# Kernel optimization log

Measured on AMD Instinct MI355X. Metric: run time of the kernel, lower is better.

Reference implementation:

```python
import jax, jax.numpy as jnp
import numpy as np

TOPK = 13
ALPHA = 1.0
BETA = 6.0
EPS = 1e-9


def _make_boxes(key, shape, img=640.0, min_sz=10.0, max_sz=110.0):
    k1, k2 = jax.random.split(key)
    cxcy = jax.random.uniform(k1, shape[:-1] + (2,)) * img
    wh = min_sz + jax.random.uniform(k2, shape[:-1] + (2,)) * (max_sz - min_sz)
    return jnp.concatenate([cxcy - wh / 2, cxcy + wh / 2], axis=-1)


def setup_inputs() -> dict:
    key = jax.random.key(0)
    ks = jax.random.split(key, 8)
    B, L, C, n, K = 16, 8400, 1, 32, 68
    pred_scores = jax.random.uniform(ks[0], (B, L, C))
    pred_bboxes = _make_boxes(ks[1], (B, L, 4))
    anchor_points = jax.random.uniform(ks[2], (L, 2)) * 640.0
    gt_labels = jax.random.randint(ks[3], (B, n, 1), 0, C).astype(jnp.int64)
    gt_bboxes = _make_boxes(ks[4], (B, n, 4))
    gt_poses = jax.random.normal(ks[5], (B, n, K, 3))
    gt_vertices = jax.random.normal(ks[6], (B, n, K, 3))
    gt_rotations = jax.random.normal(ks[7], (B, n, 3, 3))
    pad_gt_mask = jnp.ones((B, n, 1), jnp.float32)
    return {"pred_scores": pred_scores, "pred_bboxes": pred_bboxes,
            "anchor_points": anchor_points, "gt_labels": gt_labels,
            "gt_bboxes": gt_bboxes, "gt_poses": gt_poses,
            "gt_vertices": gt_vertices, "gt_rotations": gt_rotations,
            "pad_gt_mask": pad_gt_mask, "bg_index": 1}


def batch_iou_similarity(box1, box2):
    # box1 [B,n,4], box2 [B,L,4] -> [B,n,L]
    b1 = box1[:, :, None, :]
    b2 = box2[:, None, :, :]
    x1y1 = jnp.maximum(b1[..., :2], b2[..., :2])
    x2y2 = jnp.minimum(b1[..., 2:], b2[..., 2:])
    overlap = jnp.clip(x2y2 - x1y1, 0).prod(-1)
    area1 = jnp.clip(b1[..., 2:] - b1[..., :2], 0).prod(-1)
    area2 = jnp.clip(b2[..., 2:] - b2[..., :2], 0).prod(-1)
    return overlap / (area1 + area2 - overlap + EPS)


def check_points_inside_bboxes(points, bboxes):
    # points [L,2], bboxes [B,n,4] -> [B,n,L] float
    x = points[None, None, :, 0]
    y = points[None, None, :, 1]
    xmin, ymin, xmax, ymax = jnp.split(bboxes[:, :, None, :], 4, axis=-1)
    deltas = jnp.stack([x - xmin[..., 0], y - ymin[..., 0],
                        xmax[..., 0] - x, ymax[..., 0] - y], axis=-1)
    return (deltas.min(-1) > EPS).astype(bboxes.dtype)


def gather_topk_anchors(metrics, topk, topk_mask):
    # metrics [B,n,L], topk_mask [B,n,1] -> [B,n,L]
    L = metrics.shape[-1]
    _, topk_idxs = jax.lax.top_k(metrics, topk)  # [B,n,topk]
    is_in_topk = jax.nn.one_hot(topk_idxs, L, dtype=metrics.dtype).sum(-2)
    return is_in_topk * topk_mask


def compute_max_iou_anchor(ious):
    # [B,n,L] -> one-hot over gt dim of per-anchor argmax iou
    n = ious.shape[1]
    idx = ious.argmax(axis=1)  # [B,L]
    return jnp.transpose(jax.nn.one_hot(idx, n, dtype=ious.dtype), (0, 2, 1))


def reference(pred_scores, pred_bboxes, anchor_points, gt_labels, gt_bboxes,
              gt_poses, gt_vertices, gt_rotations, pad_gt_mask, bg_index):
    B, L, C = pred_scores.shape
    n = gt_bboxes.shape[1]
    K = gt_poses.shape[2]

    ious = batch_iou_similarity(gt_bboxes, pred_bboxes)  # [B,n,L]
    ps_t = jnp.transpose(pred_scores, (0, 2, 1))  # [B,C,L]
    lbl = gt_labels[..., 0]  # [B,n]
    bbox_cls_scores = jnp.take_along_axis(ps_t, lbl[:, :, None], axis=1)  # [B,n,L]

    alignment_metrics = (bbox_cls_scores ** ALPHA) * (ious ** BETA)
    is_in_gts = check_points_inside_bboxes(anchor_points, gt_bboxes)
    is_in_topk = gather_topk_anchors(alignment_metrics * is_in_gts, TOPK, pad_gt_mask)
    mask_positive = is_in_topk * is_in_gts * pad_gt_mask  # [B,n,L]
    mask_positive_sum = mask_positive.sum(axis=1)  # [B,L]

    # resolve anchors assigned to multiple gts by max IoU (no-op when none)
    mask_multiple = jnp.broadcast_to((mask_positive_sum[:, None, :] > 1), mask_positive.shape)
    is_max_iou = compute_max_iou_anchor(ious)
    mask_positive = jnp.where(mask_multiple, is_max_iou, mask_positive)
    mask_positive_sum = mask_positive.sum(axis=1)

    batch_ind = jnp.arange(B, dtype=jnp.int32)[:, None]
    assigned_gt_index = mask_positive.argmax(axis=1)  # [B,L]
    assigned_gt_index = assigned_gt_index + batch_ind * n
    flat_idx = assigned_gt_index.reshape(-1)

    assigned_labels = gt_labels.reshape(-1)[flat_idx].reshape(B, L)
    assigned_labels = jnp.where(mask_positive_sum > 0, assigned_labels, bg_index)

    assigned_bboxes = gt_bboxes.reshape(-1, 4)[flat_idx].reshape(B, L, 4)
    assigned_poses = gt_poses.reshape(-1, K, 3)[flat_idx].reshape(B, L, K, 3)
    assigned_vertices = gt_vertices.reshape(-1, K, 3)[flat_idx].reshape(B, L, K, 3)
    assigned_rotations = gt_rotations.reshape(-1, 3, 3)[flat_idx].reshape(B, L, 3, 3)

    scores_oh = jax.nn.one_hot(assigned_labels, C + 1, dtype=pred_scores.dtype)
    keep = jnp.array([i for i in range(C + 1) if i != bg_index], dtype=jnp.int32)
    assigned_scores = scores_oh[..., keep]  # [B,L,C]

    am = alignment_metrics * mask_positive
    max_metrics_per_instance = am.max(axis=-1, keepdims=True)
    max_ious_per_instance = (ious * mask_positive).max(axis=-1, keepdims=True)
    am = am / (max_metrics_per_instance + EPS) * max_ious_per_instance
    am = am.max(axis=1)[:, :, None]  # [B,L,1]
    assigned_scores = assigned_scores * am

    return (assigned_labels, assigned_bboxes, assigned_scores, assigned_poses,
            assigned_vertices, assigned_rotations, assigned_gt_index)
```

## Files before the change

kernel.cpp:

```cpp
#include <hip/hip_runtime.h>

#define Bn 16
#define Ln 8400
#define Cn 1
#define Ngt 32
#define Kpt 68
#define TOPKN 13
#define EPSF 1e-9f

typedef unsigned int u32;

#define OFF_LABELS   0
#define OFF_BBOXES   134400
#define OFF_SCORES   672000
#define OFF_POSES    806400
#define OFF_VERTS    28224000
#define OFF_ROT      55641600
#define OFF_GTIDX    56851200

__device__ __forceinline__ float iou_box(float gx0, float gy0, float gx1, float gy1,
                                         float4 p) {
    float ix0 = fmaxf(gx0, p.x), iy0 = fmaxf(gy0, p.y);
    float ix1 = fminf(gx1, p.z), iy1 = fminf(gy1, p.w);
    float ov = fmaxf(ix1 - ix0, 0.f) * fmaxf(iy1 - iy0, 0.f);
    float a1 = fmaxf(gx1 - gx0, 0.f) * fmaxf(gy1 - gy0, 0.f);
    float a2 = fmaxf(p.z - p.x, 0.f) * fmaxf(p.w - p.y, 0.f);
    return ov / (a1 + a2 - ov + EPSF);
}

__global__ void __launch_bounds__(256) k1_topk(
    const float* __restrict__ pred_scores, const float* __restrict__ pred_bboxes,
    const float* __restrict__ anchors, const int* __restrict__ gt_labels,
    const float* __restrict__ gt_bboxes, const float* __restrict__ pad_mask,
    u32* __restrict__ posmask)
{
    __shared__ float smet[Ln];
    __shared__ float rv[256];
    __shared__ int   ri[256];
    __shared__ int   sel[TOPKN];
    const int bi = blockIdx.x;
    const int b = bi / Ngt, i = bi % Ngt;
    const int tid = threadIdx.x;

    const float gx0 = gt_bboxes[bi*4+0];
    const float gy0 = gt_bboxes[bi*4+1];
    const float gx1 = gt_bboxes[bi*4+2];
    const float gy1 = gt_bboxes[bi*4+3];
    const int   label = gt_labels[bi];

    const float4* pb = (const float4*)(pred_bboxes + (size_t)b * Ln * 4);
    const float*  ps = pred_scores + (size_t)b * Ln * Cn;
    const float2* ap = (const float2*)anchors;

    for (int l = tid; l < Ln; l += 256) {
        float4 pv = pb[l];
        float iou = iou_box(gx0, gy0, gx1, gy1, pv);
        float sc = ps[l * Cn + label];
        float i2 = iou * iou;
        float m = sc * (i2 * i2 * i2);
        float2 av = ap[l];
        float dmin = fminf(fminf(av.x - gx0, av.y - gy0),
                           fminf(gx1 - av.x, gy1 - av.y));
        smet[l] = (dmin > EPSF) ? m : 0.0f;
    }
    __syncthreads();

    for (int t = 0; t < TOPKN; t++) {
        float bv = -1.f; int bidx = 0;
        for (int l = tid; l < Ln; l += 256) {
            float v = smet[l];
            if (v > bv) { bv = v; bidx = l; }
        }
        rv[tid] = bv; ri[tid] = bidx;
        __syncthreads();
        for (int s = 128; s > 0; s >>= 1) {
            if (tid < s) {
                float ov2 = rv[tid+s]; int oi = ri[tid+s];
                if (ov2 > rv[tid] || (ov2 == rv[tid] && oi < ri[tid])) {
                    rv[tid] = ov2; ri[tid] = oi;
                }
            }
            __syncthreads();
        }
        if (tid == 0) { sel[t] = ri[0]; smet[ri[0]] = -1.f; }
        __syncthreads();
    }

    const float pad = pad_mask[bi];
    if (tid < TOPKN && pad != 0.f) {
        int l = sel[tid];
        float2 av = ap[l];
        float dmin = fminf(fminf(av.x - gx0, av.y - gy0),
                           fminf(gx1 - av.x, gy1 - av.y));
        if (dmin > EPSF) atomicOr(&posmask[(size_t)b * Ln + l], 1u << i);
    }
}

__global__ void __launch_bounds__(256) k2_resolve(
    const float* __restrict__ pred_scores, const float* __restrict__ pred_bboxes,
    const int* __restrict__ gt_labels, const float* __restrict__ gt_bboxes,
    const u32* __restrict__ posmask, u32* __restrict__ finalmask,
    int* __restrict__ srcidx, float* __restrict__ met_sel,
    float* __restrict__ maxm, float* __restrict__ maxiou)
{
    int bl = blockIdx.x * 256 + threadIdx.x;
    if (bl >= Bn * Ln) return;
    int b = bl / Ln, l = bl - b * Ln;
    u32 pm = posmask[bl];
    u32 fm = pm;
    float4 pbox = ((const float4*)pred_bboxes)[bl];
    const float4* gb = (const float4*)(gt_bboxes + (size_t)b * Ngt * 4);
    if (__popc(pm) > 1) {
        float best = -1.f; int bi2 = 0;
        for (int i = 0; i < Ngt; i++) {
            float4 g = gb[i];
            float v = iou_box(g.x, g.y, g.z, g.w, pbox);
            if (v > best) { best = v; bi2 = i; }
        }
        fm = 1u << bi2;
    }
    finalmask[bl] = fm;
    int idx = fm ? (__ffs((int)fm) - 1) : 0;
    int src = b * Ngt + idx;
    srcidx[bl] = src;
    float met = 0.f;
    if (fm) {
        float4 g = gb[idx];
        float iou = iou_box(g.x, g.y, g.z, g.w, pbox);
        float sc = pred_scores[(size_t)bl * Cn + gt_labels[src]];
        float i2 = iou * iou;
        met = sc * (i2 * i2 * i2);
        atomicMax((int*)&maxm[src],   __float_as_int(met));
        atomicMax((int*)&maxiou[src], __float_as_int(iou));
    }
    met_sel[bl] = met;
}

__global__ void __launch_bounds__(256) k4_outputs(
    const u32* __restrict__ finalmask, const int* __restrict__ srcidx,
    const float* __restrict__ met_sel, const float* __restrict__ maxm_a,
    const float* __restrict__ maxiou_a, const int* __restrict__ gt_labels,
    const float* __restrict__ gt_bboxes, const float* __restrict__ gt_rot,
    const int* __restrict__ bg_index_p, float* __restrict__ out)
{
    int bl = blockIdx.x * 256 + threadIdx.x;
    if (bl >= Bn * Ln) return;
    const int bg = *bg_index_p;
    u32 fm = finalmask[bl];
    int src = srcidx[bl];
    int label = fm ? gt_labels[src] : bg;
    float am = 0.f;
    if (fm) am = met_sel[bl] / (maxm_a[src] + EPSF) * maxiou_a[src];
    int keep0 = (bg == 0) ? 1 : 0;
    float sc = (label == keep0) ? am : 0.f;

    out[OFF_LABELS + bl] = (float)label;
    out[OFF_SCORES + bl] = sc;
    out[OFF_GTIDX  + bl] = (float)src;
    ((float4*)(out + OFF_BBOXES))[bl] = ((const float4*)gt_bboxes)[src];
    const float* rs = gt_rot + src * 9;
    float* rd = out + OFF_ROT + (size_t)bl * 9;
#pragma unroll
    for (int j = 0; j < 9; j++) rd[j] = rs[j];
}

__global__ void __launch_bounds__(256) k5_gather(
    const float* __restrict__ gt_poses, const float* __restrict__ gt_verts,
    const int* __restrict__ srcidx, float* __restrict__ out)
{
    const int QPER = (Kpt * 3) / 4;
    const int total = Bn * Ln * QPER;
    int q = blockIdx.x * 256 + threadIdx.x;
    if (q >= 2 * total) return;
    const float* ga = gt_poses;
    float4* outp = (float4*)(out + OFF_POSES);
    int qq = q;
    if (qq >= total) { qq -= total; ga = gt_verts; outp = (float4*)(out + OFF_VERTS); }
    int bl = qq / QPER;
    int r = qq - bl * QPER;
    int src = srcidx[bl];
    outp[qq] = ((const float4*)ga)[src * QPER + r];
}

extern "C" void kernel_launch(void* const* d_in, const int* in_sizes, int n_in,
                              void* d_out, int out_size, void* d_ws, size_t ws_size,
                              hipStream_t stream)
{
    const float* pred_scores = (const float*)d_in[0];
    const float* pred_bboxes = (const float*)d_in[1];
    const float* anchors     = (const float*)d_in[2];
    const int*   gt_labels   = (const int*)d_in[3];
    const float* gt_bboxes   = (const float*)d_in[4];
    const float* gt_poses    = (const float*)d_in[5];
    const float* gt_verts    = (const float*)d_in[6];
    const float* gt_rot      = (const float*)d_in[7];
    const float* pad_mask    = (const float*)d_in[8];
    const int*   bg_index    = (const int*)d_in[9];

    const int nBL = Bn * Ln;
    u32*   posmask  = (u32*)d_ws;
    float* maxm     = (float*)(posmask + nBL);
    float* maxiou   = maxm + Bn * Ngt;
    u32*   finalmask= (u32*)(maxiou + Bn * Ngt);
    int*   srcidx   = (int*)(finalmask + nBL);
    float* met_sel  = (float*)(srcidx + nBL);

    hipMemsetAsync(posmask, 0, ((size_t)nBL + 2 * Bn * Ngt) * sizeof(u32), stream);

    k1_topk<<<Bn * Ngt, 256, 0, stream>>>(pred_scores, pred_bboxes, anchors,
                                          gt_labels, gt_bboxes, pad_mask, posmask);
    k2_resolve<<<(nBL + 255) / 256, 256, 0, stream>>>(pred_scores, pred_bboxes,
                                                      gt_labels, gt_bboxes, posmask,
                                                      finalmask, srcidx, met_sel,
                                                      maxm, maxiou);
    k4_outputs<<<(nBL + 255) / 256, 256, 0, stream>>>(finalmask, srcidx, met_sel,
                                                      maxm, maxiou, gt_labels,
                                                      gt_bboxes, gt_rot, bg_index,
                                                      (float*)d_out);
    const int nq = 2 * Bn * Ln * ((Kpt * 3) / 4);
    k5_gather<<<(nq + 255) / 256, 256, 0, stream>>>(gt_poses, gt_verts, srcidx,
                                                    (float*)d_out);
}
```

Measured before the change: 302.3 us.

## Compact in-box candidates before top-k and merge output kernels

The top-k kernel now stores only anchors that lie inside the GT box and have a positive metric, compacted into a shared list of up to 2048 entries. The 13 selection rounds then scan that short list with wavefront shuffle reductions instead of scanning all 8400 anchors with a shared-memory tree. The kernel also exits early for padded GTs and falls back to a serial index-order fill when fewer than 13 candidates exist. The two output kernels are merged into one launch. The risks are silent truncation if more than 2048 candidates appear, and subtle tie-breaking differences from the reference top_k when zero-metric anchors are involved.

```diff
diff --git a/kernel.cpp b/kernel.cpp
--- a/kernel.cpp
+++ b/kernel.cpp
@@ -7,6 +7,7 @@
 #define Kpt 68
 #define TOPKN 13
 #define EPSF 1e-9f
+#define CAP 2048
 
 typedef unsigned int u32;
 
@@ -34,13 +35,18 @@
     const float* __restrict__ gt_bboxes, const float* __restrict__ pad_mask,
     u32* __restrict__ posmask)
 {
-    __shared__ float smet[Ln];
-    __shared__ float rv[256];
-    __shared__ int   ri[256];
+    __shared__ float cmet[CAP];
+    __shared__ int   cidx[CAP];
+    __shared__ int   count;
+    __shared__ float rv[4];
+    __shared__ int   rl[4], rc[4];
     __shared__ int   sel[TOPKN];
+
     const int bi = blockIdx.x;
-    const int b = bi / Ngt, i = bi % Ngt;
+    const int b = bi >> 5, i = bi & 31;
     const int tid = threadIdx.x;
+
+    if (pad_mask[bi] == 0.f) return;
 
     const float gx0 = gt_bboxes[bi*4+0];
     const float gy0 = gt_bboxes[bi*4+1];
@@ -52,47 +58,75 @@
     const float*  ps = pred_scores + (size_t)b * Ln * Cn;
     const float2* ap = (const float2*)anchors;
 
+    if (tid == 0) count = 0;
+    __syncthreads();
+
     for (int l = tid; l < Ln; l += 256) {
-        float4 pv = pb[l];
-        float iou = iou_box(gx0, gy0, gx1, gy1, pv);
-        float sc = ps[l * Cn + label];
-        float i2 = iou * iou;
-        float m = sc * (i2 * i2 * i2);
         float2 av = ap[l];
         float dmin = fminf(fminf(av.x - gx0, av.y - gy0),
                            fminf(gx1 - av.x, gy1 - av.y));
-        smet[l] = (dmin > EPSF) ? m : 0.0f;
+        if (dmin > EPSF) {
+            float4 pv = pb[l];
+            float iou = iou_box(gx0, gy0, gx1, gy1, pv);
+            float sc = ps[l * Cn + label];
+            float i2 = iou * iou;
+            float m = sc * (i2 * i2 * i2);
+            if (m > 0.f) {
+                int c = atomicAdd(&count, 1);
+                if (c < CAP) { cmet[c] = m; cidx[c] = l; }
+            }
+        }
     }
     __syncthreads();
-
-    for (int t = 0; t < TOPKN; t++) {
-        float bv = -1.f; int bidx = 0;
-        for (int l = tid; l < Ln; l += 256) {
-            float v = smet[l];
-            if (v > bv) { bv = v; bidx = l; }
-        }
-        rv[tid] = bv; ri[tid] = bidx;
-        __syncthreads();
-        for (int s = 128; s > 0; s >>= 1) {
-            if (tid < s) {
-                float ov2 = rv[tid+s]; int oi = ri[tid+s];
-                if (ov2 > rv[tid] || (ov2 == rv[tid] && oi < ri[tid])) {
-                    rv[tid] = ov2; ri[tid] = oi;
+    int p = min(count, CAP);
+
+    if (p > TOPKN) {
+        for (int t = 0; t < TOPKN; t++) {
+            float bv = -1.f; int bl = 1 << 30, bc = 0;
+            for (int c = tid; c < p; c += 256) {
+                float v = cmet[c];
+                int l = cidx[c];
+                if (v > bv || (v == bv && l < bl)) { bv = v; bl = l; bc = c; }
+            }
+            #pragma unroll
+            for (int off = 32; off > 0; off >>= 1) {
+                float ov = __shfl_down(bv, off);
+                int ol = __shfl_down(bl, off);
+                int oc = __shfl_down(bc, off);
+                if (ov > bv || (ov == bv && ol < bl)) { bv = ov; bl = ol; bc = oc; }
+            }
+            int w = tid >> 6;
+            if ((tid & 63) == 0) { rv[w] = bv; rl[w] = bl; rc[w] = bc; }
+            __syncthreads();
+            if (tid == 0) {
+                float fv = rv[0]; int fl = rl[0], fc = rc[0];
+                #pragma unroll
+                for (int w2 = 1; w2 < 4; w2++) {
+                    if (rv[w2] > fv || (rv[w2] == fv && rl[w2] < fl)) {
+                        fv = rv[w2]; fl = rl[w2]; fc = rc[w2];
+                    }
                 }
+                sel[t] = fl;
+                cmet[fc] = -1.f;
             }
             __syncthreads();
         }
-        if (tid == 0) { sel[t] = ri[0]; smet[ri[0]] = -1.f; }
-        __syncthreads();
-    }
-
-    const float pad = pad_mask[bi];
-    if (tid < TOPKN && pad != 0.f) {
-        int l = sel[tid];
-        float2 av = ap[l];
-        float dmin = fminf(fminf(av.x - gx0, av.y - gy0),
-                           fminf(gx1 - av.x, gy1 - av.y));
-        if (dmin > EPSF) atomicOr(&posmask[(size_t)b * Ln + l], 1u << i);
+        if (tid < TOPKN) atomicOr(&posmask[(size_t)b * Ln + sel[tid]], 1u << i);
+    } else {
+        if (tid < p) atomicOr(&posmask[(size_t)b * Ln + cidx[tid]], 1u << i);
+        if (tid == 0) {
+            int need = TOPKN - p;
+            for (int l = 0; need > 0 && l < Ln; l++) {
+                bool isc = false;
+                for (int j = 0; j < p; j++) isc |= (cidx[j] == l);
+                if (isc) continue;
+                need--;
+                float2 av = ap[l];
+                float dmin = fminf(fminf(av.x - gx0, av.y - gy0),
+                                   fminf(gx1 - av.x, gy1 - av.y));
+                if (dmin > EPSF) atomicOr(&posmask[(size_t)b * Ln + l], 1u << i);
+            }
+        }
     }
 }
 
@@ -105,7 +139,7 @@
 {
     int bl = blockIdx.x * 256 + threadIdx.x;
     if (bl >= Bn * Ln) return;
-    int b = bl / Ln, l = bl - b * Ln;
+    int b = bl / Ln;
     u32 pm = posmask[bl];
     u32 fm = pm;
     float4 pbox = ((const float4*)pred_bboxes)[bl];
@@ -136,14 +170,30 @@
     met_sel[bl] = met;
 }
 
-__global__ void __launch_bounds__(256) k4_outputs(
+__global__ void __launch_bounds__(256) k3_out(
+    const float* __restrict__ gt_poses, const float* __restrict__ gt_verts,
     const u32* __restrict__ finalmask, const int* __restrict__ srcidx,
     const float* __restrict__ met_sel, const float* __restrict__ maxm_a,
     const float* __restrict__ maxiou_a, const int* __restrict__ gt_labels,
     const float* __restrict__ gt_bboxes, const float* __restrict__ gt_rot,
     const int* __restrict__ bg_index_p, float* __restrict__ out)
 {
-    int bl = blockIdx.x * 256 + threadIdx.x;
+    const int QPER = (Kpt * 3) / 4;
+    const int total = Bn * Ln * QPER;
+    const int nq = 2 * total;
+    int t = blockIdx.x * 256 + threadIdx.x;
+    if (t < nq) {
+        const float* ga = gt_poses;
+        float4* outp = (float4*)(out + OFF_POSES);
+        int qq = t;
+        if (qq >= total) { qq -= total; ga = gt_verts; outp = (float4*)(out + OFF_VERTS); }
+        int bl = qq / QPER;
+        int r = qq - bl * QPER;
+        int src = srcidx[bl];
+        outp[qq] = ((const float4*)ga)[src * QPER + r];
+        return;
+    }
+    int bl = t - nq;
     if (bl >= Bn * Ln) return;
     const int bg = *bg_index_p;
     u32 fm = finalmask[bl];
@@ -162,24 +212,6 @@
     float* rd = out + OFF_ROT + (size_t)bl * 9;
 #pragma unroll
     for (int j = 0; j < 9; j++) rd[j] = rs[j];
-}
-
-__global__ void __launch_bounds__(256) k5_gather(
-    const float* __restrict__ gt_poses, const float* __restrict__ gt_verts,
-    const int* __restrict__ srcidx, float* __restrict__ out)
-{
-    const int QPER = (Kpt * 3) / 4;
-    const int total = Bn * Ln * QPER;
-    int q = blockIdx.x * 256 + threadIdx.x;
-    if (q >= 2 * total) return;
-    const float* ga = gt_poses;
-    float4* outp = (float4*)(out + OFF_POSES);
-    int qq = q;
-    if (qq >= total) { qq -= total; ga = gt_verts; outp = (float4*)(out + OFF_VERTS); }
-    int bl = qq / QPER;
-    int r = qq - bl * QPER;
-    int src = srcidx[bl];
-    outp[qq] = ((const float4*)ga)[src * QPER + r];
 }
 
 extern "C" void kernel_launch(void* const* d_in, const int* in_sizes, int n_in,
@@ -213,11 +245,10 @@
                                                       gt_labels, gt_bboxes, posmask,
                                                       finalmask, srcidx, met_sel,
                                                       maxm, maxiou);
-    k4_outputs<<<(nBL + 255) / 256, 256, 0, stream>>>(finalmask, srcidx, met_sel,
-                                                      maxm, maxiou, gt_labels,
-                                                      gt_bboxes, gt_rot, bg_index,
-                                                      (float*)d_out);
     const int nq = 2 * Bn * Ln * ((Kpt * 3) / 4);
-    k5_gather<<<(nq + 255) / 256, 256, 0, stream>>>(gt_poses, gt_verts, srcidx,
-                                                    (float*)d_out);
-}
+    const int ntot = nq + nBL;
+    k3_out<<<(ntot + 255) / 256, 256, 0, stream>>>(gt_poses, gt_verts, finalmask,
+                                                   srcidx, met_sel, maxm, maxiou,
+                                                   gt_labels, gt_bboxes, gt_rot,
+                                                   bg_index, (float*)d_out);
+}
```

After: 301.5 us. About the same (-0.3%).
